# Kernel tuning notes

Measured on AMD Instinct MI355X. Metric: run time of the kernel, lower is better.

## Reference

```python
import jax, jax.numpy as jnp
import numpy as np

HID = 128
N_NODES = 50000
N_EDGES = 800000
N_GRAPHS = 64
N_LAYERS = 2
BN_EPS = 1e-5


def setup_inputs() -> dict:
    key = jax.random.key(0)
    ks = jax.random.split(key, 12)
    x_idx = jax.random.randint(ks[0], (N_NODES,), 0, 19)
    edge_index = jax.random.randint(ks[1], (2, N_EDGES), 0, N_NODES)
    edge_attr = jax.random.randint(ks[2], (N_EDGES,), 0, 4)
    batch = jnp.sort(jax.random.randint(ks[3], (N_NODES,), 0, N_GRAPHS))
    s = 1.0 / np.sqrt(HID)
    node_emb = jax.random.normal(ks[4], (19, HID), jnp.float32)
    edge_emb = jax.random.normal(ks[5], (4, HID), jnp.float32)
    # stacked per-layer GINE MLP params: Linear->ReLU->Linear->ReLU->BN
    W1 = jax.random.uniform(ks[6], (N_LAYERS, HID, HID), jnp.float32, -s, s)
    b1 = jnp.zeros((N_LAYERS, HID), jnp.float32)
    W2 = jax.random.uniform(ks[7], (N_LAYERS, HID, HID), jnp.float32, -s, s)
    b2 = jnp.zeros((N_LAYERS, HID), jnp.float32)
    bn_g = jnp.ones((N_LAYERS, HID), jnp.float32)
    bn_b = jnp.zeros((N_LAYERS, HID), jnp.float32)
    return {"x_idx": x_idx, "edge_index": edge_index, "edge_attr": edge_attr,
            "batch": batch, "node_emb": node_emb, "edge_emb": edge_emb,
            "W1": W1, "b1": b1, "W2": W2, "b2": b2, "bn_g": bn_g, "bn_b": bn_b}


def _gine_layer(x, e_feat, src, dst, W1, b1, W2, b2, g, beta):
    # GINEConv (eps=0): nn(x + sum_{j->i} relu(x_j + e_ji))
    msg = jax.nn.relu(x[src] + e_feat)                       # [E, H] gather
    aggr = jax.ops.segment_sum(msg, dst, num_segments=x.shape[0])  # scatter-add
    h = x + aggr
    h = jax.nn.relu(h @ W1 + b1)
    h = jax.nn.relu(h @ W2 + b2)
    mu = h.mean(0)
    var = h.var(0)
    return g * (h - mu) * jax.lax.rsqrt(var + BN_EPS) + beta  # training-mode BN


def reference(x_idx, edge_index, edge_attr, batch, node_emb, edge_emb,
              W1, b1, W2, b2, bn_g, bn_b):
    x = node_emb[x_idx]                 # [N, H]
    e_feat = edge_emb[edge_attr]        # [E, H] (encoded once, shared by layers)
    src, dst = edge_index[0], edge_index[1]
    for l in range(N_LAYERS):
        x = _gine_layer(x, e_feat, src, dst, W1[l], b1[l], W2[l], b2[l], bn_g[l], bn_b[l])
    pooled = jax.ops.segment_sum(x, batch, num_segments=N_GRAPHS)  # global_add_pool
    return pooled
```

## Files before the change

kernel.cpp:

```cpp
#include <hip/hip_runtime.h>
#include <hip/hip_bf16.h>

#define HID 128
#define NNODES 50000
#define NEDGES 800000
#define NGRAPHS 64
#define BN_EPS 1e-5f
#define CAP 64

#define SENTW 0x009C0000

typedef __attribute__((ext_vector_type(8))) short short8;
typedef __attribute__((ext_vector_type(4))) float f32x4;

static __device__ __forceinline__ unsigned short f2bf(float v) {
  __hip_bfloat16 b = __float2bfloat16(v);
  return *reinterpret_cast<unsigned short*>(&b);
}
static __device__ __forceinline__ float bf2f(unsigned short u) {
  return __uint_as_float(((unsigned)u) << 16);
}
static __device__ __forceinline__ float lo16f(unsigned u) {
  return __uint_as_float(u << 16);
}
static __device__ __forceinline__ float hi16f(unsigned u) {
  return __uint_as_float(u & 0xFFFF0000u);
}

static __device__ __forceinline__ unsigned packhl(float v) {
  unsigned short h = f2bf(v);
  unsigned short l = f2bf(v - bf2f(h));
  return (unsigned)h | ((unsigned)l << 16);
}
static __device__ __forceinline__ float upk(unsigned p) {
  return __uint_as_float(p << 16) + __uint_as_float(p & 0xFFFF0000u);
}
static __device__ __forceinline__ void unpack8(uint4 wa, uint4 wb,
                                               short8& hi, short8& lo) {
  union U { unsigned u[4]; short8 s; };
  U H, L;
  unsigned w[8] = {wa.x, wa.y, wa.z, wa.w, wb.x, wb.y, wb.z, wb.w};
  #pragma unroll
  for (int t = 0; t < 4; t++) {
    unsigned a = w[2 * t], b = w[2 * t + 1];
    H.u[t] = (a & 0xFFFFu) | (b << 16);
    L.u[t] = (a >> 16) | (b & 0xFFFF0000u);
  }
  hi = H.s; lo = L.s;
}

__global__ __launch_bounds__(256) void prep_kernel(
    const int* __restrict__ x_idx, const float* __restrict__ node_emb,
    const int* __restrict__ eidx, const int* __restrict__ eattr,
    int* __restrict__ cnt, int* __restrict__ eout,
    const float* __restrict__ W1, const float* __restrict__ W2,
    unsigned short* __restrict__ Wpk, unsigned* __restrict__ msgTg,
    unsigned* __restrict__ typeT, const float* __restrict__ edge_emb) {
  int i = blockIdx.x * 256 + threadIdx.x;
  int stride = gridDim.x * 256;
  for (int e = i; e < NEDGES; e += stride) {
    int s = eidx[e];
    int d = eidx[NEDGES + e];
    int ty = x_idx[s];
    int pos = atomicAdd(&cnt[d], 1);
    if (pos < CAP)
      eout[((size_t)d << 6) + pos] = s | (eattr[e] << 16) | (ty << 19);
  }
  for (int idx = i; idx < 77 * 64; idx += stride) {
    int combo = idx >> 6, c2 = (idx & 63) << 1;
    unsigned v = 0;
    if (combo < 76) {
      int ty = combo >> 2, at = combo & 3;
      float a0 = fmaxf(node_emb[ty * HID + c2] + edge_emb[at * HID + c2], 0.f);
      float a1 = fmaxf(node_emb[ty * HID + c2 + 1] + edge_emb[at * HID + c2 + 1], 0.f);
      v = (unsigned)f2bf(a0) | ((unsigned)f2bf(a1) << 16);
    }
    msgTg[idx] = v;
  }
  for (int idx = i; idx < 19 * 64; idx += stride) {
    int ty = idx >> 6, c2 = (idx & 63) << 1;
    typeT[idx] = (unsigned)f2bf(node_emb[ty * HID + c2]) |
                 ((unsigned)f2bf(node_emb[ty * HID + c2 + 1]) << 16);
  }
  for (int idx = i; idx < 65536; idx += stride) {
    int j = idx & 7;
    int l = (idx >> 3) & 63;
    int q = (idx >> 9) & 3;
    int t = (idx >> 11) & 7;
    int m = idx >> 14;
    int k = ((l >> 4) << 3) + j + (q << 5);
    int n = (t << 4) + (l & 15);
    int layer = m >> 1;
    const float* W = (m & 1) ? W2 : W1;
    float w = W[(size_t)layer * HID * HID + k * HID + n];
    unsigned short h = f2bf(w);
    Wpk[idx] = h;
    Wpk[idx + 65536] = f2bf(w - bf2f(h));
  }
}

#define NT 32
#define LDAF 132
#define GRID_GINE ((NNODES + NT - 1) / NT)

template <bool L0>
__global__ __launch_bounds__(512, 8) void gine_mlp_kernel(
    const unsigned short* __restrict__ in_bf,
    const int* __restrict__ xidx,
    const float* __restrict__ instats,
    const float* __restrict__ gam, const float* __restrict__ bet,
    const int* __restrict__ cnt, const int* __restrict__ eout,
    const unsigned* __restrict__ msgTg, const float* __restrict__ edge_emb,
    const short8* __restrict__ Wh, const short8* __restrict__ Wl,
    const float* __restrict__ b1, const float* __restrict__ b2,
    unsigned short* __restrict__ out_bf, float* __restrict__ stats,
    const int* __restrict__ batch, float* __restrict__ gpool) {
  extern __shared__ __align__(16) char smem[];
  unsigned* hAp = (unsigned*)smem;
  float* sheL = (float*)(smem + NT * LDAF * 4);
  float* red = (float*)(smem + NT * LDAF * 4);
  const int tid = threadIdx.x;
  const int lane = tid & 63;
  const int wave = tid >> 6;
  const int base = blockIdx.x * NT;

  float scl_lo = 1.0f, scl_hi = 1.0f, sh_lo = 0.0f, sh_hi = 0.0f;

  if constexpr (!L0) {
    if (tid < 4 * HID) {
      int c = tid & 127;
      float mu = instats[c] * (1.0f / NNODES);
      float var = instats[HID + c] * (1.0f / NNODES) - mu * mu;
      float s = gam[c] * rsqrtf(var + BN_EPS);
      float shc = bet[c] - mu * s;
      sheL[tid] = shc + edge_emb[tid];
    }
    if (tid < HID) sheL[4 * HID + tid] = -1e30f;
    {
      int c0 = lane << 1;
      float mu0 = instats[c0] * (1.0f / NNODES);
      float var0 = instats[HID + c0] * (1.0f / NNODES) - mu0 * mu0;
      scl_lo = gam[c0] * rsqrtf(var0 + BN_EPS);
      sh_lo = bet[c0] - mu0 * scl_lo;
      float mu1 = instats[c0 + 1] * (1.0f / NNODES);
      float var1 = instats[HID + c0 + 1] * (1.0f / NNODES) - mu1 * mu1;
      scl_hi = gam[c0 + 1] * rsqrtf(var1 + BN_EPS);
      sh_hi = bet[c0 + 1] - mu1 * scl_hi;
    }
    __syncthreads();
  }

  {
    const unsigned* in4 = (const unsigned*)in_bf;
    int node0 = base + wave * 4;
    float acc0[4], acc1[4];
    #pragma unroll
    for (int i = 0; i < 4; i++) { acc0[i] = 0.0f; acc1[i] = 0.0f; }

    int dg4[4], epw4[4];
    unsigned sv4[4];
    #pragma unroll
    for (int i = 0; i < 4; i++) {
      int node = node0 + i;
      bool v = node < NNODES;
      dg4[i] = v ? __builtin_amdgcn_readfirstlane(min(cnt[node], CAP)) : 0;
      epw4[i] = v ? eout[(node << 6) + lane] : 0;
      epw4[i] = (lane < dg4[i]) ? epw4[i] : SENTW;
      int srow;
      if constexpr (L0)
        srow = v ? __builtin_amdgcn_readfirstlane(xidx[node]) : 0;
      else
        srow = node;
      sv4[i] = v ? in4[(srow << 6) + lane] : 0u;
    }

#define GL_ISSUE(SB, X, A)                                      \
    {                                                           \
      _Pragma("unroll")                                         \
      for (int jj = 0; jj < 8; jj++) {                          \
        int w = __builtin_amdgcn_readlane(epw, (SB) + jj);      \
        A[jj] = (w >> 16) & 7;                                  \
        X[jj] = in4[((w & 0xFFFF) << 6) + lane];                \
      }                                                         \
    }
#define GL_CONS(X, A)                                           \
    {                                                           \
      _Pragma("unroll")                                         \
      for (int jj = 0; jj < 8; jj++) {                          \
        float2 e2 = *(const float2*)&sheL[(A[jj] << 7) + (lane << 1)]; \
        acc0[i] += fmaxf(fmaf(lo16f(X[jj]), scl_lo, e2.x), 0.0f); \
        acc1[i] += fmaxf(fmaf(hi16f(X[jj]), scl_hi, e2.y), 0.0f); \
      }                                                         \
    }
#define GT_ISSUE(SB, M)                                         \
    {                                                           \
      _Pragma("unroll")                                         \
      for (int jj = 0; jj < 8; jj++) {                          \
        int w = __builtin_amdgcn_readlane(epw, (SB) + jj);      \
        int combo = ((w >> 17) & 124) | ((w >> 16) & 3);        \
        M[jj] = msgTg[(combo << 6) + lane];                     \
      }                                                         \
    }
#define GT_CONS(M)                                              \
    {                                                           \
      _Pragma("unroll")                                         \
      for (int jj = 0; jj < 8; jj++) {                          \
        acc0[i] += lo16f(M[jj]);                                \
        acc1[i] += hi16f(M[jj]);                                \
      }                                                         \
    }

    #pragma unroll
    for (int i = 0; i < 4; i++) {
      int node = node0 + i;
      if (node >= NNODES) continue;
      int dg = dg4[i];
      int dgR = (dg + 7) & ~7;
      int epw = epw4[i];
      if constexpr (L0) {
        acc0[i] = lo16f(sv4[i]);
        acc1[i] = hi16f(sv4[i]);
      } else {
        acc0[i] = fmaf(lo16f(sv4[i]), scl_lo, sh_lo);
        acc1[i] = fmaf(hi16f(sv4[i]), scl_hi, sh_hi);
      }
      if (dgR > 0) {
        if constexpr (L0) {
          unsigned M0[8], M1[8];
          GT_ISSUE(0, M0);
          int sb = 0;
          for (;;) {
            if (sb + 8 < dgR) GT_ISSUE(sb + 8, M1);
            GT_CONS(M0);
            sb += 8;
            if (sb >= dgR) break;
            if (sb + 8 < dgR) GT_ISSUE(sb + 8, M0);
            GT_CONS(M1);
            sb += 8;
            if (sb >= dgR) break;
          }
        } else {
          unsigned X0[8], X1[8];
          int A0[8], A1[8];
          GL_ISSUE(0, X0, A0);
          int sb = 0;
          for (;;) {
            if (sb + 8 < dgR) GL_ISSUE(sb + 8, X1, A1);
            GL_CONS(X0, A0);
            sb += 8;
            if (sb >= dgR) break;
            if (sb + 8 < dgR) GL_ISSUE(sb + 8, X0, A0);
            GL_CONS(X1, A1);
            sb += 8;
            if (sb >= dgR) break;
          }
        }
      }
    }
#undef GL_ISSUE
#undef GL_CONS
#undef GT_ISSUE
#undef GT_CONS

    #pragma unroll
    for (int i = 0; i < 4; i++) {
      int nrow = wave * 4 + i;
      hAp[nrow * LDAF + (lane << 1)] = packhl(acc0[i]);
      hAp[nrow * LDAF + (lane << 1) + 1] = packhl(acc1[i]);
    }
  }
  __syncthreads();

  const int col = lane & 15;
  const int quad = lane >> 4;
  const int rbase = quad * 4;
  const int ch0 = wave * 16 + col;
  const int aoff = quad * 8;

  {
    f32x4 a0 = {0.f, 0.f, 0.f, 0.f}, a1 = a0;
    #pragma unroll
    for (int q = 0; q < 4; q++) {
      int f0 = wave * 256 + q * 64 + lane;
      short8 b0h = Wh[f0], b0l = Wl[f0];
      const unsigned* r0 = &hAp[col * LDAF + q * 32 + aoff];
      const unsigned* r1 = &hAp[(16 + col) * LDAF + q * 32 + aoff];
      short8 a0h, a0l, a1h, a1l;
      unpack8(*(const uint4*)r0, *(const uint4*)(r0 + 4), a0h, a0l);
      unpack8(*(const uint4*)r1, *(const uint4*)(r1 + 4), a1h, a1l);
      a0 = __builtin_amdgcn_mfma_f32_16x16x32_bf16(a0h, b0h, a0, 0, 0, 0);
      a0 = __builtin_amdgcn_mfma_f32_16x16x32_bf16(a0l, b0h, a0, 0, 0, 0);
      a0 = __builtin_amdgcn_mfma_f32_16x16x32_bf16(a0h, b0l, a0, 0, 0, 0);
      a1 = __builtin_amdgcn_mfma_f32_16x16x32_bf16(a1h, b0h, a1, 0, 0, 0);
      a1 = __builtin_amdgcn_mfma_f32_16x16x32_bf16(a1l, b0h, a1, 0, 0, 0);
      a1 = __builtin_amdgcn_mfma_f32_16x16x32_bf16(a1h, b0l, a1, 0, 0, 0);
    }
    __syncthreads();
    float bb0 = b1[ch0];
    #pragma unroll
    for (int r = 0; r < 4; r++) {
      hAp[(rbase + r) * LDAF + ch0] = packhl(fmaxf(a0[r] + bb0, 0.0f));
      hAp[(16 + rbase + r) * LDAF + ch0] = packhl(fmaxf(a1[r] + bb0, 0.0f));
    }
  }
  __syncthreads();

  {
    f32x4 a0 = {0.f, 0.f, 0.f, 0.f}, a1 = a0;
    #pragma unroll
    for (int q = 0; q < 4; q++) {
      int f0 = 2048 + wave * 256 + q * 64 + lane;
      short8 b0h = Wh[f0], b0l = Wl[f0];
      const unsigned* r0 = &hAp[col * LDAF + q * 32 + aoff];
      const unsigned* r1 = &hAp[(16 + col) * LDAF + q * 32 + aoff];
      short8 a0h, a0l, a1h, a1l;
      unpack8(*(const uint4*)r0, *(const uint4*)(r0 + 4), a0h, a0l);
      unpack8(*(const uint4*)r1, *(const uint4*)(r1 + 4), a1h, a1l);
      a0 = __builtin_amdgcn_mfma_f32_16x16x32_bf16(a0h, b0h, a0, 0, 0, 0);
      a0 = __builtin_amdgcn_mfma_f32_16x16x32_bf16(a0l, b0h, a0, 0, 0, 0);
      a0 = __builtin_amdgcn_mfma_f32_16x16x32_bf16(a0h, b0l, a0, 0, 0, 0);
      a1 = __builtin_amdgcn_mfma_f32_16x16x32_bf16(a1h, b0h, a1, 0, 0, 0);
      a1 = __builtin_amdgcn_mfma_f32_16x16x32_bf16(a1l, b0h, a1, 0, 0, 0);
      a1 = __builtin_amdgcn_mfma_f32_16x16x32_bf16(a1h, b0l, a1, 0, 0, 0);
    }
    __syncthreads();
    float bb0 = b2[ch0];
    #pragma unroll
    for (int r = 0; r < 4; r++) {
      hAp[(rbase + r) * LDAF + ch0] = packhl(fmaxf(a0[r] + bb0, 0.0f));
      hAp[(16 + rbase + r) * LDAF + ch0] = packhl(fmaxf(a1[r] + bb0, 0.0f));
    }
  }
  __syncthreads();

  float lsum = 0.0f, lsq = 0.0f;
  if (tid < 256) {
    const int c = tid & 127;
    const int yy = tid >> 7;
    if (out_bf) {
      #pragma unroll 4
      for (int i = 0; i < 16; i++) {
        int n = yy * 16 + i;
        int node = base + n;
        if (node < NNODES) {
          unsigned p = hAp[n * LDAF + c];
          out_bf[node * HID + c] = (unsigned short)(p & 0xFFFF);
          float v = upk(p);
          lsum += v;
          lsq += v * v;
        }
      }
    } else {
      int curg = -1;
      float pacc = 0.0f;
      for (int i = 0; i < 16; i++) {
        int n = yy * 16 + i;
        int node = base + n;
        if (node < NNODES) {
          float v = upk(hAp[n * LDAF + c]);
          lsum += v;
          lsq += v * v;
          int bg = batch[node];
          if (bg != curg) {
            if (curg >= 0) unsafeAtomicAdd(&gpool[curg * HID + c], pacc);
            curg = bg;
            pacc = 0.0f;
          }
          pacc += v;
        }
      }
      if (curg >= 0) unsafeAtomicAdd(&gpool[curg * HID + c], pacc);
    }
    if (tid >= 128) {
      red[tid - 128] = lsum;
      red[tid] = lsq;
    }
  }
  __syncthreads();
  if (tid < 128) {
    lsum += red[tid];
    lsq += red[128 + tid];
    unsafeAtomicAdd(&stats[tid], lsum);
    unsafeAtomicAdd(&stats[HID + tid], lsq);
  }
}

__device__ __forceinline__ int lbound(const int* __restrict__ arr, int n,
                                      int key) {
  int lo = 0, hi = n;
  while (lo < hi) {
    int mid = (lo + hi) >> 1;
    if (arr[mid] < key) lo = mid + 1; else hi = mid;
  }
  return lo;
}

__global__ __launch_bounds__(128) void finish_kernel(
    const float* __restrict__ gpool, const float* __restrict__ stats,
    const float* __restrict__ gam, const float* __restrict__ bet,
    const int* __restrict__ batch, float* __restrict__ out) {
  __shared__ int cnt_s;
  int g = blockIdx.x, c = threadIdx.x;
  if (c == 0)
    cnt_s = lbound(batch, NNODES, g + 1) - lbound(batch, NNODES, g);
  __syncthreads();
  float mu = stats[c] * (1.0f / NNODES);
  float var = stats[HID + c] * (1.0f / NNODES) - mu * mu;
  float scl = gam[c] * rsqrtf(var + BN_EPS);
  float sh = bet[c] - mu * scl;
  out[g * HID + c] = fmaf(gpool[g * HID + c], scl, (float)cnt_s * sh);
}

extern "C" void kernel_launch(void* const* d_in, const int* in_sizes, int n_in,
                              void* d_out, int out_size, void* d_ws, size_t ws_size,
                              hipStream_t stream) {
  const int* x_idx = (const int*)d_in[0];
  const int* eidx = (const int*)d_in[1];
  const int* eattr = (const int*)d_in[2];
  const int* batch = (const int*)d_in[3];
  const float* node_emb = (const float*)d_in[4];
  const float* edge_emb = (const float*)d_in[5];
  const float* W1 = (const float*)d_in[6];
  const float* b1 = (const float*)d_in[7];
  const float* W2 = (const float*)d_in[8];
  const float* b2 = (const float*)d_in[9];
  const float* bn_g = (const float*)d_in[10];
  const float* bn_b = (const float*)d_in[11];
  float* out = (float*)d_out;

  const size_t nfeat = (size_t)NNODES * HID;
  unsigned short* h2bf = (unsigned short*)d_ws;
  float* stats0 = (float*)(h2bf + nfeat);
  float* stats1 = stats0 + 2 * HID;
  float* gpool = stats1 + 2 * HID;
  int* cnt = (int*)(gpool + NGRAPHS * HID);
  int* eout = cnt + NNODES;
  unsigned short* Wpk = (unsigned short*)(eout + (size_t)NNODES * CAP);
  unsigned* msgTg = (unsigned*)(Wpk + 131072);
  unsigned* typeT = msgTg + 77 * 64;
  size_t needed = (size_t)((char*)(typeT + 19 * 64) - (char*)d_ws);
  if (ws_size < needed) return;

  hipMemsetAsync(stats0, 0, (4 * HID + NGRAPHS * HID + NNODES) * sizeof(int),
                 stream);

  prep_kernel<<<3125, 256, 0, stream>>>(x_idx, node_emb, eidx, eattr, cnt,
                                        eout, W1, W2, Wpk, msgTg, typeT,
                                        edge_emb);

  const short8* Wfh = (const short8*)Wpk;
  const short8* Wfl = Wfh + 8192;
  const size_t smemsz = (size_t)NT * LDAF * 4 + 5 * HID * 4;
  gine_mlp_kernel<true><<<GRID_GINE, 512, smemsz, stream>>>(
      (const unsigned short*)typeT, x_idx, nullptr, nullptr, nullptr, cnt,
      eout, msgTg, edge_emb, Wfh + 0 * 2048, Wfl + 0 * 2048, b1, b2, h2bf,
      stats0, nullptr, nullptr);
  gine_mlp_kernel<false><<<GRID_GINE, 512, smemsz, stream>>>(
      h2bf, nullptr, stats0, bn_g, bn_b, cnt, eout, msgTg, edge_emb,
      Wfh + 2 * 2048, Wfl + 2 * 2048, b1 + HID, b2 + HID, nullptr, stats1,
      batch, gpool);
  finish_kernel<<<NGRAPHS, 128, 0, stream>>>(gpool, stats1, bn_g + HID,
                                             bn_b + HID, batch, out);
}
```

Baseline: 265.1 us.

## Flatten per-node gather loops into a triple-buffered software pipeline across nodes

Replaces the per-node double-buffered gather loops with a single fully unrolled, triple-buffered schedule over 32 eight-edge chunks covering all four nodes of a wave. Loads for the next chunks, including those of the following node, are issued before the current chunk is consumed, so memory latency is hidden across node boundaries. Edge-attribute indices are packed into one register to save VGPRs. The cost is much larger code, predicated chunk checks, and more register pressure from three live buffers.

```diff
diff --git a/kernel.cpp b/kernel.cpp
--- a/kernel.cpp
+++ b/kernel.cpp
@@ -154,11 +154,7 @@
     const unsigned* in4 = (const unsigned*)in_bf;
     int node0 = base + wave * 4;
     float acc0[4], acc1[4];
-    #pragma unroll
-    for (int i = 0; i < 4; i++) { acc0[i] = 0.0f; acc1[i] = 0.0f; }
-
     int dg4[4], epw4[4];
-    unsigned sv4[4];
     #pragma unroll
     for (int i = 0; i < 4; i++) {
       int node = node0 + i;
@@ -171,96 +167,134 @@
         srow = v ? __builtin_amdgcn_readfirstlane(xidx[node]) : 0;
       else
         srow = node;
-      sv4[i] = v ? in4[(srow << 6) + lane] : 0u;
-    }
-
-#define GL_ISSUE(SB, X, A)                                      \
-    {                                                           \
-      _Pragma("unroll")                                         \
-      for (int jj = 0; jj < 8; jj++) {                          \
-        int w = __builtin_amdgcn_readlane(epw, (SB) + jj);      \
-        A[jj] = (w >> 16) & 7;                                  \
-        X[jj] = in4[((w & 0xFFFF) << 6) + lane];                \
-      }                                                         \
-    }
-#define GL_CONS(X, A)                                           \
-    {                                                           \
-      _Pragma("unroll")                                         \
-      for (int jj = 0; jj < 8; jj++) {                          \
-        float2 e2 = *(const float2*)&sheL[(A[jj] << 7) + (lane << 1)]; \
-        acc0[i] += fmaxf(fmaf(lo16f(X[jj]), scl_lo, e2.x), 0.0f); \
-        acc1[i] += fmaxf(fmaf(hi16f(X[jj]), scl_hi, e2.y), 0.0f); \
-      }                                                         \
-    }
-#define GT_ISSUE(SB, M)                                         \
-    {                                                           \
-      _Pragma("unroll")                                         \
-      for (int jj = 0; jj < 8; jj++) {                          \
-        int w = __builtin_amdgcn_readlane(epw, (SB) + jj);      \
-        int combo = ((w >> 17) & 124) | ((w >> 16) & 3);        \
-        M[jj] = msgTg[(combo << 6) + lane];                     \
-      }                                                         \
-    }
-#define GT_CONS(M)                                              \
-    {                                                           \
-      _Pragma("unroll")                                         \
-      for (int jj = 0; jj < 8; jj++) {                          \
-        acc0[i] += lo16f(M[jj]);                                \
-        acc1[i] += hi16f(M[jj]);                                \
-      }                                                         \
-    }
-
-    #pragma unroll
-    for (int i = 0; i < 4; i++) {
-      int node = node0 + i;
-      if (node >= NNODES) continue;
-      int dg = dg4[i];
-      int dgR = (dg + 7) & ~7;
-      int epw = epw4[i];
+      unsigned sv = v ? in4[(srow << 6) + lane] : 0u;
       if constexpr (L0) {
-        acc0[i] = lo16f(sv4[i]);
-        acc1[i] = hi16f(sv4[i]);
+        acc0[i] = lo16f(sv);
+        acc1[i] = hi16f(sv);
       } else {
-        acc0[i] = fmaf(lo16f(sv4[i]), scl_lo, sh_lo);
-        acc1[i] = fmaf(hi16f(sv4[i]), scl_hi, sh_hi);
+        acc0[i] = v ? fmaf(lo16f(sv), scl_lo, sh_lo) : 0.0f;
+        acc1[i] = v ? fmaf(hi16f(sv), scl_hi, sh_hi) : 0.0f;
       }
-      if (dgR > 0) {
-        if constexpr (L0) {
-          unsigned M0[8], M1[8];
-          GT_ISSUE(0, M0);
-          int sb = 0;
-          for (;;) {
-            if (sb + 8 < dgR) GT_ISSUE(sb + 8, M1);
-            GT_CONS(M0);
-            sb += 8;
-            if (sb >= dgR) break;
-            if (sb + 8 < dgR) GT_ISSUE(sb + 8, M0);
-            GT_CONS(M1);
-            sb += 8;
-            if (sb >= dgR) break;
-          }
-        } else {
-          unsigned X0[8], X1[8];
-          int A0[8], A1[8];
-          GL_ISSUE(0, X0, A0);
-          int sb = 0;
-          for (;;) {
-            if (sb + 8 < dgR) GL_ISSUE(sb + 8, X1, A1);
-            GL_CONS(X0, A0);
-            sb += 8;
-            if (sb >= dgR) break;
-            if (sb + 8 < dgR) GL_ISSUE(sb + 8, X0, A0);
-            GL_CONS(X1, A1);
-            sb += 8;
-            if (sb >= dgR) break;
-          }
-        }
-      }
-    }
-#undef GL_ISSUE
-#undef GL_CONS
-#undef GT_ISSUE
-#undef GT_CONS
+    }
+
+#define VLD(K) (((((K) & 7)) << 3) < dg4[(K) >> 3])
+#define I1(K, X, AW)                                                    \
+    if (VLD(K)) {                                                       \
+      AW = 0u;                                                          \
+      _Pragma("unroll")                                                 \
+      for (int jj = 0; jj < 8; jj++) {                                  \
+        int w = __builtin_amdgcn_readlane(epw4[(K) >> 3],               \
+                                          (((K) & 7) << 3) + jj);       \
+        AW |= (unsigned)((w >> 16) & 7) << (3 * jj);                    \
+        X[jj] = in4[((w & 0xFFFF) << 6) + lane];                        \
+      }                                                                 \
+    }
+#define C1(K, X, AW)                                                    \
+    if (VLD(K)) {                                                       \
+      _Pragma("unroll")                                                 \
+      for (int jj = 0; jj < 8; jj++) {                                  \
+        int at = (int)((AW >> (3 * jj)) & 7);                           \
+        float2 e2 = *(const float2*)&sheL[(at << 7) + (lane << 1)];     \
+        acc0[(K) >> 3] += fmaxf(fmaf(lo16f(X[jj]), scl_lo, e2.x), 0.0f); \
+        acc1[(K) >> 3] += fmaxf(fmaf(hi16f(X[jj]), scl_hi, e2.y), 0.0f); \
+      }                                                                 \
+    }
+#define I0(K, M)                                                        \
+    if (VLD(K)) {                                                       \
+      _Pragma("unroll")                                                 \
+      for (int jj = 0; jj < 8; jj++) {                                  \
+        int w = __builtin_amdgcn_readlane(epw4[(K) >> 3],               \
+                                          (((K) & 7) << 3) + jj);       \
+        int combo = ((w >> 17) & 124) | ((w >> 16) & 3);                \
+        M[jj] = msgTg[(combo << 6) + lane];                             \
+      }                                                                 \
+    }
+#define C0(K, M)                                                        \
+    if (VLD(K)) {                                                       \
+      _Pragma("unroll")                                                 \
+      for (int jj = 0; jj < 8; jj++) {                                  \
+        acc0[(K) >> 3] += lo16f(M[jj]);                                 \
+        acc1[(K) >> 3] += hi16f(M[jj]);                                 \
+      }                                                                 \
+    }
+
+    if constexpr (L0) {
+      unsigned Ma[8], Mb[8], Mc[8];
+      I0(0, Ma)
+      I0(1, Mb)
+      I0(2, Mc) C0(0, Ma)
+      I0(3, Ma) C0(1, Mb)
+      I0(4, Mb) C0(2, Mc)
+      I0(5, Mc) C0(3, Ma)
+      I0(6, Ma) C0(4, Mb)
+      I0(7, Mb) C0(5, Mc)
+      I0(8, Mc) C0(6, Ma)
+      I0(9, Ma) C0(7, Mb)
+      I0(10, Mb) C0(8, Mc)
+      I0(11, Mc) C0(9, Ma)
+      I0(12, Ma) C0(10, Mb)
+      I0(13, Mb) C0(11, Mc)
+      I0(14, Mc) C0(12, Ma)
+      I0(15, Ma) C0(13, Mb)
+      I0(16, Mb) C0(14, Mc)
+      I0(17, Mc) C0(15, Ma)
+      I0(18, Ma) C0(16, Mb)
+      I0(19, Mb) C0(17, Mc)
+      I0(20, Mc) C0(18, Ma)
+      I0(21, Ma) C0(19, Mb)
+      I0(22, Mb) C0(20, Mc)
+      I0(23, Mc) C0(21, Ma)
+      I0(24, Ma) C0(22, Mb)
+      I0(25, Mb) C0(23, Mc)
+      I0(26, Mc) C0(24, Ma)
+      I0(27, Ma) C0(25, Mb)
+      I0(28, Mb) C0(26, Mc)
+      I0(29, Mc) C0(27, Ma)
+      I0(30, Ma) C0(28, Mb)
+      I0(31, Mb) C0(29, Mc)
+      C0(30, Ma) C0(31, Mb)
+    } else {
+      unsigned Xa[8], Xb[8], Xc[8];
+      unsigned awa, awb, awc;
+      I1(0, Xa, awa)
+      I1(1, Xb, awb)
+      I1(2, Xc, awc) C1(0, Xa, awa)
+      I1(3, Xa, awa) C1(1, Xb, awb)
+      I1(4, Xb, awb) C1(2, Xc, awc)
+      I1(5, Xc, awc) C1(3, Xa, awa)
+      I1(6, Xa, awa) C1(4, Xb, awb)
+      I1(7, Xb, awb) C1(5, Xc, awc)
+      I1(8, Xc, awc) C1(6, Xa, awa)
+      I1(9, Xa, awa) C1(7, Xb, awb)
+      I1(10, Xb, awb) C1(8, Xc, awc)
+      I1(11, Xc, awc) C1(9, Xa, awa)
+      I1(12, Xa, awa) C1(10, Xb, awb)
+      I1(13, Xb, awb) C1(11, Xc, awc)
+      I1(14, Xc, awc) C1(12, Xa, awa)
+      I1(15, Xa, awa) C1(13, Xb, awb)
+      I1(16, Xb, awb) C1(14, Xc, awc)
+      I1(17, Xc, awc) C1(15, Xa, awa)
+      I1(18, Xa, awa) C1(16, Xb, awb)
+      I1(19, Xb, awb) C1(17, Xc, awc)
+      I1(20, Xc, awc) C1(18, Xa, awa)
+      I1(21, Xa, awa) C1(19, Xb, awb)
+      I1(22, Xb, awb) C1(20, Xc, awc)
+      I1(23, Xc, awc) C1(21, Xa, awa)
+      I1(24, Xa, awa) C1(22, Xb, awb)
+      I1(25, Xb, awb) C1(23, Xc, awc)
+      I1(26, Xc, awc) C1(24, Xa, awa)
+      I1(27, Xa, awa) C1(25, Xb, awb)
+      I1(28, Xb, awb) C1(26, Xc, awc)
+      I1(29, Xc, awc) C1(27, Xa, awa)
+      I1(30, Xa, awa) C1(28, Xb, awb)
+      I1(31, Xb, awb) C1(29, Xc, awc)
+      C1(30, Xa, awa) C1(31, Xb, awb)
+    }
+#undef VLD
+#undef I1
+#undef C1
+#undef I0
+#undef C0
 
     #pragma unroll
     for (int i = 0; i < 4; i++) {
```

Measured after the change: 259.1 us. -2.2%, faster.
